# Kernel optimization log

Hardware: AMD Instinct MI355X
Metric: run time of the kernel (lower is better)

The kernel has to match this reference:

```python
import jax, jax.numpy as jnp
import numpy as np

N = 50000   # nodes
E = 800000  # edges
D_FEAT = 128
D_HID = 128
D_EMB = 128


def _xavier(key, shape):
    fan_in, fan_out = shape
    lim = float(np.sqrt(6.0 / (fan_in + fan_out)))
    return jax.random.uniform(key, shape, jnp.float32, -lim, lim)


def setup_inputs() -> dict:
    key = jax.random.key(0)
    ks = jax.random.split(key, 12)
    return {
        "x": jax.random.normal(ks[0], (N, D_FEAT), jnp.float32),
        "edge_index": jax.random.randint(ks[1], (2, E), 0, N),
        "x_aug": jax.random.normal(ks[2], (N, D_FEAT), jnp.float32),
        "edge_index_aug": jax.random.randint(ks[3], (2, E), 0, N),
        # GCNConv weights (PyG stores lin.weight [out,in]; we use [in,out])
        "W_in": _xavier(ks[4], (D_FEAT, D_HID)),
        "b_in": jnp.zeros((D_HID,), jnp.float32),
        "W_h": _xavier(ks[5], (D_HID, D_HID)),
        "b_h": jnp.zeros((D_HID,), jnp.float32),
        "W_out": _xavier(ks[6], (D_HID, D_EMB)),
        "b_out": jnp.zeros((D_EMB,), jnp.float32),
        # fc head: Linear(embed,hidden) -> ReLU -> Linear(hidden,embed)
        "Wf1": _xavier(ks[7], (D_EMB, D_HID)),
        "bf1": jnp.zeros((D_HID,), jnp.float32),
        "Wf2": _xavier(ks[8], (D_HID, D_EMB)),
        "bf2": jnp.zeros((D_EMB,), jnp.float32),
    }


def gcn_layer(x, W, b, src, dst):
    """GCNConv: out = D^{-1/2}(A+I)D^{-1/2} (x @ W) + b, deg counted with self-loops."""
    n = x.shape[0]
    h = x @ W                                    # [N, out]
    deg = jax.ops.segment_sum(jnp.ones(src.shape[0], x.dtype), dst, num_segments=n) + 1.0
    dis = jax.lax.rsqrt(deg)                      # deg >= 1 due to self-loop
    norm = dis[src] * dis[dst]                    # [E]
    agg = jax.ops.segment_sum(h[src] * norm[:, None], dst, num_segments=n)
    agg = agg + h * (dis * dis)[:, None]          # self-loop contribution
    return agg + b


def gcn_forward(x, edge_index, W_in, b_in, W_h, b_h, W_out, b_out, Wf1, bf1, Wf2, bf2):
    src, dst = edge_index[0], edge_index[1]
    x = jax.nn.relu(gcn_layer(x, W_in, b_in, src, dst))
    # dropout(p=0.5, training=False) is identity in eval mode
    x = jax.nn.relu(gcn_layer(x, W_h, b_h, src, dst))
    x = jax.nn.relu(gcn_layer(x, W_out, b_out, src, dst))
    x = jax.nn.relu(x @ Wf1 + bf1) @ Wf2 + bf2
    return x


def reference(x, edge_index, x_aug, edge_index_aug, W_in, b_in, W_h, b_h,
              W_out, b_out, Wf1, bf1, Wf2, bf2):
    out = gcn_forward(x, edge_index, W_in, b_in, W_h, b_h, W_out, b_out, Wf1, bf1, Wf2, bf2)
    out_aug = gcn_forward(x_aug, edge_index_aug, W_in, b_in, W_h, b_h, W_out, b_out, Wf1, bf1, Wf2, bf2)
    return (out, out_aug)
```

## Files before the change

kernel.cpp:

```cpp
#include <hip/hip_runtime.h>
#include <hip/hip_bf16.h>

#define D 128

typedef __bf16 bf16x8 __attribute__((ext_vector_type(8)));
typedef float  f32x4  __attribute__((ext_vector_type(4)));


__global__ void k_count_deg2(const int* __restrict__ ei, const int* __restrict__ eia,
                             int* __restrict__ deg, int e0, int e1, int n0) {
    int i = blockIdx.x * blockDim.x + threadIdx.x;
    if (i < e0) atomicAdd(&deg[ei[e0 + i]], 1);
    else if (i < e0 + e1) { int k = i - e0; atomicAdd(&deg[eia[e1 + k] + n0], 1); }
}

__global__ void k_dis(const int* __restrict__ deg, float* __restrict__ dis, int n) {
    int i = blockIdx.x * blockDim.x + threadIdx.x;
    if (i < n) dis[i] = rsqrtf((float)deg[i] + 1.0f);
}

__global__ __launch_bounds__(256) void k_scan1(const int* __restrict__ deg,
                                               int* __restrict__ rowptr,
                                               int* __restrict__ bsum, int n) {
    __shared__ int tmp[256];
    int t = threadIdx.x;
    int i = blockIdx.x * 256 + t;
    tmp[t] = (i < n) ? deg[i] : 0;
    __syncthreads();
    for (int ofs = 1; ofs < 256; ofs <<= 1) {
        int add = (t >= ofs) ? tmp[t - ofs] : 0;
        __syncthreads();
        tmp[t] += add;
        __syncthreads();
    }
    if (i < n) rowptr[i + 1] = tmp[t];
    if (t == 255) bsum[blockIdx.x] = tmp[255];
}

__global__ __launch_bounds__(256) void k_scan2(int* __restrict__ bsum, int nb) {
    __shared__ int tmp[256];
    int t = threadIdx.x;
    int carry = 0;
    for (int base = 0; base < nb; base += 256) {
        int idx = base + t;
        tmp[t] = (idx < nb) ? bsum[idx] : 0;
        __syncthreads();
        for (int ofs = 1; ofs < 256; ofs <<= 1) {
            int add = (t >= ofs) ? tmp[t - ofs] : 0;
            __syncthreads();
            tmp[t] += add;
            __syncthreads();
        }
        if (idx < nb) bsum[idx] = tmp[t] + carry;
        int total = tmp[255];
        __syncthreads();
        carry += total;
    }
}

__global__ void k_scan3(int* __restrict__ rowptr, int* __restrict__ cursor,
                        const int* __restrict__ bsum, int n) {
    int i = blockIdx.x * blockDim.x + threadIdx.x;
    if (i == 0) { rowptr[0] = 0; cursor[0] = 0; }
    if (i < n) {
        int b = i >> 8;
        int val = rowptr[i + 1];
        if (b > 0) val += bsum[b - 1];
        rowptr[i + 1] = val;
        if (i + 1 < n) cursor[i + 1] = val;
    }
}

__global__ void k_csr_fill2(const int* __restrict__ ei, const int* __restrict__ eia,
                            int* __restrict__ cursor, int* __restrict__ csr_src,
                            int e0, int e1, int n0) {
    int i = blockIdx.x * blockDim.x + threadIdx.x;
    int s, d;
    if (i < e0) { s = ei[i]; d = ei[e0 + i]; }
    else if (i < e0 + e1) { int k = i - e0; s = eia[k]; d = eia[e1 + k] + n0; }
    else return;
    int pos = atomicAdd(&cursor[d], 1);
    csr_src[pos] = s;
}


__global__ __launch_bounds__(256) void k_pack_w5(
    const float* __restrict__ w0, const float* __restrict__ w1,
    const float* __restrict__ w2, const float* __restrict__ w3,
    const float* __restrict__ w4, __bf16* __restrict__ out) {
    int q = blockIdx.x >> 6;
    const float* W = (q == 0) ? w0 : (q == 1) ? w1 : (q == 2) ? w2 : (q == 3) ? w3 : w4;
    int i = ((blockIdx.x & 63) << 8) | threadIdx.x;
    int j    = i & 7;
    int lane = (i >> 3) & 63;
    int ct   = (i >> 9) & 7;
    int kb   = i >> 12;
    int k = kb * 32 + (lane >> 4) * 8 + j;
    int c = ct * 16 + (lane & 15);
    float w = W[k * D + c];
    __bf16 hi = (__bf16)w;
    __bf16 lo = (__bf16)(w - (float)hi);
    __bf16* dstp = out + (size_t)q * 32768;
    dstp[i] = hi;
    dstp[16384 + i] = lo;
}


__global__ __launch_bounds__(256) void k_gemm_mfma(
    const float* __restrict__ A, const __bf16* __restrict__ Wp,
    const float* __restrict__ bias, float* __restrict__ C, int n,
    int fuse_bias, int fuse_relu) {
    __shared__ __bf16 Ws[32768];
    int t = threadIdx.x;
    for (int i = t * 8; i < 32768; i += 2048)
        *(float4*)&Ws[i] = *(const float4*)&Wp[i];

    int wv = t >> 6, lane = t & 63;
    int lrow = lane & 15, lhi = lane >> 4;
    int m0 = blockIdx.x * 64 + wv * 16;

    bf16x8 ahi[4], alo[4];
    int arow = m0 + lrow;
    const float* ap = A + (size_t)arow * D + lhi * 8;
    #pragma unroll
    for (int kb = 0; kb < 4; ++kb) {
        float av[8];
        if (arow < n) {
            float4 p0 = *(const float4*)(ap + kb * 32);
            float4 p1 = *(const float4*)(ap + kb * 32 + 4);
            av[0] = p0.x; av[1] = p0.y; av[2] = p0.z; av[3] = p0.w;
            av[4] = p1.x; av[5] = p1.y; av[6] = p1.z; av[7] = p1.w;
        } else {
            #pragma unroll
            for (int j = 0; j < 8; ++j) av[j] = 0.0f;
        }
        #pragma unroll
        for (int j = 0; j < 8; ++j) {
            __bf16 h = (__bf16)av[j];
            ahi[kb][j] = h;
            alo[kb][j] = (__bf16)(av[j] - (float)h);
        }
    }
    __syncthreads();

    f32x4 acc[8];
    f32x4 zz = {0.f, 0.f, 0.f, 0.f};
    #pragma unroll
    for (int i = 0; i < 8; ++i) acc[i] = zz;

    #pragma unroll
    for (int kb = 0; kb < 4; ++kb) {
        #pragma unroll
        for (int ct = 0; ct < 8; ++ct) {
            int off = ((kb * 8 + ct) * 64 + lane) * 8;
            bf16x8 bh = *(const bf16x8*)&Ws[off];
            bf16x8 bl = *(const bf16x8*)&Ws[16384 + off];
            acc[ct] = __builtin_amdgcn_mfma_f32_16x16x32_bf16(ahi[kb], bh, acc[ct], 0, 0, 0);
            acc[ct] = __builtin_amdgcn_mfma_f32_16x16x32_bf16(ahi[kb], bl, acc[ct], 0, 0, 0);
            acc[ct] = __builtin_amdgcn_mfma_f32_16x16x32_bf16(alo[kb], bh, acc[ct], 0, 0, 0);
        }
    }

    #pragma unroll
    for (int ct = 0; ct < 8; ++ct) {
        int col = ct * 16 + lrow;
        float bv = fuse_bias ? bias[col] : 0.0f;
        #pragma unroll
        for (int r = 0; r < 4; ++r) {
            int row = m0 + lhi * 4 + r;
            if (row < n) {
                float v = acc[ct][r] + bv;
                if (fuse_relu) v = fmaxf(v, 0.0f);
                C[(size_t)row * D + col] = v;
            }
        }
    }
}


__global__ __launch_bounds__(256) void k_csr_agg2(
    const float* __restrict__ H, const int* __restrict__ rowptr,
    const int* __restrict__ csr_src, const float* __restrict__ dis,
    const float* __restrict__ bias, float* __restrict__ X, int n, int relu) {
    int wid = (blockIdx.x * 256 + threadIdx.x) >> 6;
    int lane = threadIdx.x & 63;
    int w = __builtin_amdgcn_readfirstlane(wid);
    int v = w >> 1;
    int half = w & 1;
    if (v >= n) return;
    int ch = half * 64 + lane;
    float dv = dis[v];
    float acc = H[(size_t)v * D + ch] * dv * dv;
    int beg = rowptr[v], end = rowptr[v + 1];
    int j = beg;
    for (; j + 8 <= end; j += 8) {
        int s[8]; float ww[8]; float a[8];
        #pragma unroll
        for (int q = 0; q < 8; ++q) s[q] = csr_src[j + q];
        #pragma unroll
        for (int q = 0; q < 8; ++q) ww[q] = dis[s[q]] * dv;
        #pragma unroll
        for (int q = 0; q < 8; ++q) a[q] = H[(size_t)s[q] * D + ch];
        #pragma unroll
        for (int q = 0; q < 8; ++q) acc = fmaf(a[q], ww[q], acc);
    }
    for (; j < end; ++j) {
        int s = csr_src[j];
        acc = fmaf(H[(size_t)s * D + ch], dis[s] * dv, acc);
    }
    acc += bias[ch];
    if (relu) acc = fmaxf(acc, 0.f);
    X[(size_t)v * D + ch] = acc;
}


extern "C" void kernel_launch(void* const* d_in, const int* in_sizes, int n_in,
                              void* d_out, int out_size, void* d_ws, size_t ws_size,
                              hipStream_t stream) {
    const float* x    = (const float*)d_in[0];
    const int*   ei   = (const int*)d_in[1];
    const float* xa   = (const float*)d_in[2];
    const int*   eia  = (const int*)d_in[3];
    const float* W_in = (const float*)d_in[4];
    const float* b_in = (const float*)d_in[5];
    const float* W_h  = (const float*)d_in[6];
    const float* b_h  = (const float*)d_in[7];
    const float* W_out= (const float*)d_in[8];
    const float* b_out= (const float*)d_in[9];
    const float* Wf1  = (const float*)d_in[10];
    const float* bf1  = (const float*)d_in[11];
    const float* Wf2  = (const float*)d_in[12];
    const float* bf2  = (const float*)d_in[13];

    const int n0 = in_sizes[0] / D;
    const int e0 = in_sizes[1] / 2;
    const int n1 = in_sizes[2] / D;
    const int e1 = in_sizes[3] / 2;
    const int nt = n0 + n1;
    const int et = e0 + e1;

    float* Xf     = (float*)d_ws;
    float* H      = Xf + (size_t)n0 * D;
    float* dis    = H  + (size_t)n0 * D;
    int*   deg    = (int*)(dis + nt);
    int*   rowptr = deg + nt;
    int*   cursor = rowptr + (nt + 4);
    int*   bsum   = cursor + nt;
    int*   csrsrc = bsum + 512;
    __bf16* wpack = (__bf16*)(csrsrc + et);

    float* out = (float*)d_out;

    const float* bl[3] = {b_in, b_h, b_out};

    const int threads = 256;
    const int g_nt   = (nt + threads - 1) / threads;
    const int g_et   = (et + threads - 1) / threads;
    const int g_gemm = (n0 + 63) / 64;
    const int g_agg  = (n0 * 2 * 64 + threads - 1) / threads;
    const int nb     = g_nt;

    k_pack_w5<<<320, threads, 0, stream>>>(W_in, W_h, W_out, Wf1, Wf2, wpack);

    hipMemsetAsync(deg, 0, (size_t)nt * sizeof(int), stream);
    k_count_deg2<<<g_et, threads, 0, stream>>>(ei, eia, deg, e0, e1, n0);
    k_dis<<<g_nt, threads, 0, stream>>>(deg, dis, nt);
    k_scan1<<<g_nt, threads, 0, stream>>>(deg, rowptr, bsum, nt);
    k_scan2<<<1, threads, 0, stream>>>(bsum, nb);
    k_scan3<<<g_nt, threads, 0, stream>>>(rowptr, cursor, bsum, nt);
    k_csr_fill2<<<g_et, threads, 0, stream>>>(ei, eia, cursor, csrsrc, e0, e1, n0);

    for (int g = 0; g < 2; ++g) {
        const float* xin   = g ? xa : x;
        const int*   rpg   = rowptr + (size_t)g * n0;
        const float* disg  = dis + (size_t)g * n0;
        float* outg = out + (size_t)g * n0 * D;

        for (int l = 0; l < 3; ++l) {
            const float* Ain = (l == 0) ? xin : Xf;
            k_gemm_mfma<<<g_gemm, threads, 0, stream>>>(Ain, wpack + (size_t)l * 32768,
                                                        nullptr, H, n0, 0, 0);
            k_csr_agg2<<<g_agg, threads, 0, stream>>>(H, rpg, csrsrc, disg, bl[l], Xf, n0, 1);
        }

        k_gemm_mfma<<<g_gemm, threads, 0, stream>>>(Xf, wpack + (size_t)3 * 32768,
                                                    bf1, H, n0, 1, 1);
        k_gemm_mfma<<<g_gemm, threads, 0, stream>>>(H, wpack + (size_t)4 * 32768,
                                                    bf2, outg, n0, 1, 0);
    }
}
```

Baseline: 960.8 us.

## Precompute per-edge source norms and process each node with one wave

A new kernel stores dis[src] for every CSR edge in a csrw array, in CSR order. The aggregation then reads it contiguously instead of doing a dependent random gather of dis[s]. The aggregation kernel now gives each node one wave that covers all 128 channels with two accumulators, rather than two waves of 64 channels. This halves the redundant reads of the index and weight arrays, at the cost of fewer waves in flight and a shorter unroll of 4 edges. The degree-count and CSR-fill kernels also handle 4 edges per thread to cut the launch grid size.

```diff
diff --git a/kernel.cpp b/kernel.cpp
--- a/kernel.cpp
+++ b/kernel.cpp
@@ -9,9 +9,13 @@
 
 __global__ void k_count_deg2(const int* __restrict__ ei, const int* __restrict__ eia,
                              int* __restrict__ deg, int e0, int e1, int n0) {
-    int i = blockIdx.x * blockDim.x + threadIdx.x;
-    if (i < e0) atomicAdd(&deg[ei[e0 + i]], 1);
-    else if (i < e0 + e1) { int k = i - e0; atomicAdd(&deg[eia[e1 + k] + n0], 1); }
+    int base = (blockIdx.x * blockDim.x + threadIdx.x) * 4;
+    #pragma unroll
+    for (int q = 0; q < 4; ++q) {
+        int i = base + q;
+        if (i < e0) atomicAdd(&deg[ei[e0 + i]], 1);
+        else if (i < e0 + e1) { int k = i - e0; atomicAdd(&deg[eia[e1 + k] + n0], 1); }
+    }
 }
 
 __global__ void k_dis(const int* __restrict__ deg, float* __restrict__ dis, int n) {
@@ -74,13 +78,26 @@
 __global__ void k_csr_fill2(const int* __restrict__ ei, const int* __restrict__ eia,
                             int* __restrict__ cursor, int* __restrict__ csr_src,
                             int e0, int e1, int n0) {
+    int base = (blockIdx.x * blockDim.x + threadIdx.x) * 4;
+    #pragma unroll
+    for (int q = 0; q < 4; ++q) {
+        int i = base + q;
+        int s, d;
+        if (i < e0) { s = ei[i]; d = ei[e0 + i]; }
+        else if (i < e0 + e1) { int k = i - e0; s = eia[k]; d = eia[e1 + k] + n0; }
+        else continue;
+        int pos = atomicAdd(&cursor[d], 1);
+        csr_src[pos] = s;
+    }
+}
+
+__global__ void k_fill_w(const int* __restrict__ csr_src, const float* __restrict__ dis,
+                         float* __restrict__ csrw, int e0, int et, int n0) {
     int i = blockIdx.x * blockDim.x + threadIdx.x;
-    int s, d;
-    if (i < e0) { s = ei[i]; d = ei[e0 + i]; }
-    else if (i < e0 + e1) { int k = i - e0; s = eia[k]; d = eia[e1 + k] + n0; }
-    else return;
-    int pos = atomicAdd(&cursor[d], 1);
-    csr_src[pos] = s;
+    if (i < et) {
+        int s = csr_src[i];
+        csrw[i] = dis[i < e0 ? s : s + n0];
+    }
 }
 
 
@@ -178,39 +195,51 @@
 }
 
 
-__global__ __launch_bounds__(256) void k_csr_agg2(
+__global__ __launch_bounds__(256) void k_csr_agg3(
     const float* __restrict__ H, const int* __restrict__ rowptr,
-    const int* __restrict__ csr_src, const float* __restrict__ dis,
-    const float* __restrict__ bias, float* __restrict__ X, int n, int relu) {
+    const int* __restrict__ csr_src, const float* __restrict__ csrw,
+    const float* __restrict__ dis, const float* __restrict__ bias,
+    float* __restrict__ X, int n, int relu) {
     int wid = (blockIdx.x * 256 + threadIdx.x) >> 6;
     int lane = threadIdx.x & 63;
-    int w = __builtin_amdgcn_readfirstlane(wid);
-    int v = w >> 1;
-    int half = w & 1;
+    int v = __builtin_amdgcn_readfirstlane(wid);
     if (v >= n) return;
-    int ch = half * 64 + lane;
     float dv = dis[v];
-    float acc = H[(size_t)v * D + ch] * dv * dv;
+    const float* Hv = H + (size_t)v * D;
+    float acc0 = Hv[lane] * dv * dv;
+    float acc1 = Hv[lane + 64] * dv * dv;
     int beg = rowptr[v], end = rowptr[v + 1];
     int j = beg;
-    for (; j + 8 <= end; j += 8) {
-        int s[8]; float ww[8]; float a[8];
-        #pragma unroll
-        for (int q = 0; q < 8; ++q) s[q] = csr_src[j + q];
-        #pragma unroll
-        for (int q = 0; q < 8; ++q) ww[q] = dis[s[q]] * dv;
-        #pragma unroll
-        for (int q = 0; q < 8; ++q) a[q] = H[(size_t)s[q] * D + ch];
-        #pragma unroll
-        for (int q = 0; q < 8; ++q) acc = fmaf(a[q], ww[q], acc);
+    for (; j + 4 <= end; j += 4) {
+        int s0 = csr_src[j + 0], s1 = csr_src[j + 1];
+        int s2 = csr_src[j + 2], s3 = csr_src[j + 3];
+        float w0 = csrw[j + 0] * dv, w1 = csrw[j + 1] * dv;
+        float w2 = csrw[j + 2] * dv, w3 = csrw[j + 3] * dv;
+        const float* p0 = H + (size_t)s0 * D;
+        const float* p1 = H + (size_t)s1 * D;
+        const float* p2 = H + (size_t)s2 * D;
+        const float* p3 = H + (size_t)s3 * D;
+        float a0 = p0[lane], b0 = p0[lane + 64];
+        float a1 = p1[lane], b1 = p1[lane + 64];
+        float a2 = p2[lane], b2 = p2[lane + 64];
+        float a3 = p3[lane], b3 = p3[lane + 64];
+        acc0 = fmaf(a0, w0, acc0); acc1 = fmaf(b0, w0, acc1);
+        acc0 = fmaf(a1, w1, acc0); acc1 = fmaf(b1, w1, acc1);
+        acc0 = fmaf(a2, w2, acc0); acc1 = fmaf(b2, w2, acc1);
+        acc0 = fmaf(a3, w3, acc0); acc1 = fmaf(b3, w3, acc1);
     }
     for (; j < end; ++j) {
         int s = csr_src[j];
-        acc = fmaf(H[(size_t)s * D + ch], dis[s] * dv, acc);
-    }
-    acc += bias[ch];
-    if (relu) acc = fmaxf(acc, 0.f);
-    X[(size_t)v * D + ch] = acc;
+        float w = csrw[j] * dv;
+        const float* p = H + (size_t)s * D;
+        acc0 = fmaf(p[lane], w, acc0);
+        acc1 = fmaf(p[lane + 64], w, acc1);
+    }
+    acc0 += bias[lane];
+    acc1 += bias[lane + 64];
+    if (relu) { acc0 = fmaxf(acc0, 0.f); acc1 = fmaxf(acc1, 0.f); }
+    X[(size_t)v * D + lane] = acc0;
+    X[(size_t)v * D + lane + 64] = acc1;
 }
 
 
@@ -247,7 +276,8 @@
     int*   cursor = rowptr + (nt + 4);
     int*   bsum   = cursor + nt;
     int*   csrsrc = bsum + 512;
-    __bf16* wpack = (__bf16*)(csrsrc + et);
+    float* csrw   = (float*)(csrsrc + et);
+    __bf16* wpack = (__bf16*)(csrw + et);
 
     float* out = (float*)d_out;
 
@@ -256,19 +286,21 @@
     const int threads = 256;
     const int g_nt   = (nt + threads - 1) / threads;
     const int g_et   = (et + threads - 1) / threads;
+    const int g_et4  = (et + threads * 4 - 1) / (threads * 4);
     const int g_gemm = (n0 + 63) / 64;
-    const int g_agg  = (n0 * 2 * 64 + threads - 1) / threads;
+    const int g_agg  = (n0 * 64 + threads - 1) / threads;
     const int nb     = g_nt;
 
     k_pack_w5<<<320, threads, 0, stream>>>(W_in, W_h, W_out, Wf1, Wf2, wpack);
 
     hipMemsetAsync(deg, 0, (size_t)nt * sizeof(int), stream);
-    k_count_deg2<<<g_et, threads, 0, stream>>>(ei, eia, deg, e0, e1, n0);
+    k_count_deg2<<<g_et4, threads, 0, stream>>>(ei, eia, deg, e0, e1, n0);
     k_dis<<<g_nt, threads, 0, stream>>>(deg, dis, nt);
     k_scan1<<<g_nt, threads, 0, stream>>>(deg, rowptr, bsum, nt);
     k_scan2<<<1, threads, 0, stream>>>(bsum, nb);
     k_scan3<<<g_nt, threads, 0, stream>>>(rowptr, cursor, bsum, nt);
-    k_csr_fill2<<<g_et, threads, 0, stream>>>(ei, eia, cursor, csrsrc, e0, e1, n0);
+    k_csr_fill2<<<g_et4, threads, 0, stream>>>(ei, eia, cursor, csrsrc, e0, e1, n0);
+    k_fill_w<<<g_et, threads, 0, stream>>>(csrsrc, dis, csrw, e0, et, n0);
 
     for (int g = 0; g < 2; ++g) {
         const float* xin   = g ? xa : x;
@@ -280,7 +312,8 @@
             const float* Ain = (l == 0) ? xin : Xf;
             k_gemm_mfma<<<g_gemm, threads, 0, stream>>>(Ain, wpack + (size_t)l * 32768,
                                                         nullptr, H, n0, 0, 0);
-            k_csr_agg2<<<g_agg, threads, 0, stream>>>(H, rpg, csrsrc, disg, bl[l], Xf, n0, 1);
+            k_csr_agg3<<<g_agg, threads, 0, stream>>>(H, rpg, csrsrc, csrw, disg,
+                                                      bl[l], Xf, n0, 1);
         }
 
         k_gemm_mfma<<<g_gemm, threads, 0, stream>>>(Xf, wpack + (size_t)3 * 32768,
```

After: 914.5 us. 4.8% less time.
